# Kernel tuning notes

Hardware: AMD Instinct MI355X
Metric: run time of the kernel (lower is better)

## Reference

```python
import jax, jax.numpy as jnp
import numpy as np
import math

H = 16
D_MODEL = 1024
D_K = D_MODEL // H


def setup_inputs() -> dict:
    key = jax.random.key(0)
    ks = jax.random.split(key, 11)
    B, S = 2, 2048
    scale = 1.0 / math.sqrt(D_MODEL)
    inp = {
        "query": jax.random.normal(ks[0], (B, S, D_MODEL), dtype=jnp.float32),
        "key": jax.random.normal(ks[1], (B, S, D_MODEL), dtype=jnp.float32),
        "value": jax.random.normal(ks[2], (B, S, D_MODEL), dtype=jnp.float32),
        # torch nn.Linear convention: W is [out_features, in_features]
        "Wq": jax.random.normal(ks[3], (D_MODEL, D_MODEL), dtype=jnp.float32) * scale,
        "bq": jnp.zeros((D_MODEL,), dtype=jnp.float32),
        "Wk": jax.random.normal(ks[4], (D_MODEL, D_MODEL), dtype=jnp.float32) * scale,
        "bk": jnp.zeros((D_MODEL,), dtype=jnp.float32),
        "Wv": jax.random.normal(ks[5], (D_MODEL, D_MODEL), dtype=jnp.float32) * scale,
        "bv": jnp.zeros((D_MODEL,), dtype=jnp.float32),
        "Wo": jax.random.normal(ks[6], (D_MODEL, D_MODEL), dtype=jnp.float32) * scale,
        "bo": jnp.zeros((D_MODEL,), dtype=jnp.float32),
    }
    return inp


def _split_heads(x):
    # [b, s, h*d_k] -> [b, h, s, d_k]
    b, s, _ = x.shape
    return x.reshape(b, s, H, D_K).transpose(0, 2, 1, 3)


def reference(query, key, value, Wq, bq, Wk, bk, Wv, bv, Wo, bo):
    q = _split_heads(query @ Wq.T + bq)
    k = _split_heads(key @ Wk.T + bk)
    v = _split_heads(value @ Wv.T + bv)
    # scaled dot-product attention, full L x L scores per head
    scores = jnp.einsum("bhqd,bhkd->bhqk", q, k) / math.sqrt(D_K)
    attn = jax.nn.softmax(scores, axis=-1)
    ctx = jnp.einsum("bhqk,bhkd->bhqd", attn, v)  # [b, h, s, d_k]
    b, h, s, d = ctx.shape
    ctx = ctx.transpose(0, 2, 1, 3).reshape(b, s, h * d)
    return ctx @ Wo.T + bo
```

## Files before the change

### kernel.cpp

```cpp
#include <hip/hip_runtime.h>

typedef unsigned int u32;
typedef unsigned short u16;
typedef __attribute__((ext_vector_type(8))) short short8;
typedef __attribute__((ext_vector_type(4))) float f32x4;
typedef __attribute__((ext_vector_type(2))) u32 u32x2;
typedef __attribute__((ext_vector_type(4))) u32 u32x4;

#define DEV __device__ __forceinline__

DEV u16 f2bf(float f) {
  u32 u = __builtin_bit_cast(u32, f);
  u = (u + 0x7FFFu + ((u >> 16) & 1u)) >> 16;
  return (u16)u;
}

DEV float fexp2(float x) {
#if __has_builtin(__builtin_amdgcn_exp2f)
  return __builtin_amdgcn_exp2f(x);
#else
  return exp2f(x);
#endif
}

DEV u32 cvt_pk_bf16(float lo, float hi) {
  u32 r;
  asm("v_cvt_pk_bf16_f32 %0, %1, %2" : "=v"(r) : "v"(lo), "v"(hi));
  return r;
}

DEV void llds16(const void* g, void* lds) {
  __builtin_amdgcn_global_load_lds(
      (const __attribute__((address_space(1))) u32*)g,
      (__attribute__((address_space(3))) u32*)lds, 16, 0, 0);
}

struct CvtArgs {
  const float* src[7];
  u16* dst[7];
};

__global__ void cvt_all(CvtArgs ca) {
  int i = blockIdx.x * blockDim.x + threadIdx.x;
  int chunk = i >> 17;
  int seg = chunk < 12 ? (chunk >> 2) : (chunk - 9);
  u32 base8 = (seg < 3) ? (u32)seg * 524288u : 1572864u + ((u32)seg - 3) * 131072u;
  size_t off = ((size_t)i - base8) * 8;
  const f32x4* p = (const f32x4*)(ca.src[seg] + off);
  f32x4 a = p[0], b = p[1];
  short8 o;
  o[0] = (short)f2bf(a[0]); o[1] = (short)f2bf(a[1]);
  o[2] = (short)f2bf(a[2]); o[3] = (short)f2bf(a[3]);
  o[4] = (short)f2bf(b[0]); o[5] = (short)f2bf(b[1]);
  o[6] = (short)f2bf(b[2]); o[7] = (short)f2bf(b[3]);
  *(short8*)(ca.dst[seg] + off) = o;
}

struct GemmArgs {
  const u16* A[3];
  const u16* W[3];
  const float* bias[3];
  void* C[3];
  float scale[3];
};

template <int BM, int BN, int WAVES_M, int OUT_BF16, int NB_M>
__global__ __launch_bounds__(256, 2) void gemm_bt(GemmArgs ga) {
  constexpr int K = 1024, N = 1024;
  constexpr int WAVES_N = 4 / WAVES_M;
  constexpr int WM = BM / WAVES_M, WN = BN / WAVES_N;
  constexpr int AM = WM / 16, AN = WN / 16;
  constexpr int SEGS = (BM + BN) / 16;
  constexpr int PW = SEGS / 4;

  __shared__ u16 lsA[BM * 32];
  __shared__ u16 lsB[BN * 32];

  const u32 orig = blockIdx.x;
  const u32 nid = (orig & 7u) * (gridDim.x >> 3) + (orig >> 3);
  const int bn = (int)(nid & 7u);
  const int bm = (int)((nid >> 3) % (u32)NB_M);
  const int z = (int)((nid >> 3) / (u32)NB_M);

  const u16* __restrict__ A = ga.A[z];
  const u16* __restrict__ W = ga.W[z];
  const int tid = threadIdx.x;
  const int l = tid & 63, w = tid >> 6;
  const int lg = l >> 4, lr = l & 15;
  const int wm = w / WAVES_N, wn = w % WAVES_N;

  f32x4 acc[AM][AN];
#pragma unroll
  for (int i = 0; i < AM; ++i)
#pragma unroll
    for (int j = 0; j < AN; ++j) acc[i][j] = (f32x4){0.f, 0.f, 0.f, 0.f};

  for (int k0 = 0; k0 < K; k0 += 32) {
    __syncthreads();
#pragma unroll
    for (int i = 0; i < PW; ++i) {
      int s = w * PW + i;
      if (s < BM / 16) {
        u32 sb = s * 1024;
        u32 lb = sb + l * 16;
        u32 row = lb >> 6, colS = (lb & 63) >> 1;
        llds16(A + (size_t)(bm * BM + row) * K + k0 + colS, (char*)lsA + sb);
      } else {
        u32 sb = (u32)(s - BM / 16) * 1024;
        u32 lb = sb + l * 16;
        u32 row = lb >> 6, colS = (lb & 63) >> 1;
        llds16(W + (size_t)(bn * BN + row) * K + k0 + colS, (char*)lsB + sb);
      }
    }
    __syncthreads();
    short8 af[AM], bf[AN];
#pragma unroll
    for (int i = 0; i < AM; ++i)
      af[i] = *(const short8*)&lsA[(wm * WM + i * 16 + lr) * 32 + lg * 8];
#pragma unroll
    for (int j = 0; j < AN; ++j)
      bf[j] = *(const short8*)&lsB[(wn * WN + j * 16 + lr) * 32 + lg * 8];
#pragma unroll
    for (int i = 0; i < AM; ++i)
#pragma unroll
      for (int j = 0; j < AN; ++j)
        acc[i][j] = __builtin_amdgcn_mfma_f32_16x16x32_bf16(af[i], bf[j], acc[i][j], 0, 0, 0);
  }

  const float sc = ga.scale[z];
  const float* __restrict__ bias = ga.bias[z];
#pragma unroll
  for (int j = 0; j < AN; ++j) {
    int col = bn * BN + wn * WN + j * 16 + lr;
    float bv = bias[col];
#pragma unroll
    for (int i = 0; i < AM; ++i) {
      int row0 = bm * BM + wm * WM + i * 16 + lg * 4;
#pragma unroll
      for (int r = 0; r < 4; ++r) {
        float v = (acc[i][j][r] + bv) * sc;
        if constexpr (OUT_BF16)
          ((u16*)ga.C[z])[(size_t)(row0 + r) * N + col] = f2bf(v);
        else
          ((float*)ga.C[z])[(size_t)(row0 + r) * N + col] = v;
      }
    }
  }
}

__global__ __launch_bounds__(256, 2) void attn_fwd(
    const u16* __restrict__ Q, const u16* __restrict__ Kp,
    const u16* __restrict__ V, u16* __restrict__ O) {
  constexpr int S = 2048, LD = 1024;
  __shared__ u16 Kt[2][64 * 64];
  __shared__ u16 Vt[2][64 * 64];
  const int tid = threadIdx.x;
  const int l = tid & 63, w = tid >> 6;
  const int lg = l >> 4, lr = l & 15;

  const u32 orig = blockIdx.x;
  const u32 nid = (orig & 7u) * 64u + (orig >> 3);
  const int qt = (int)(nid & 15u);
  const int h = (int)((nid >> 4) & 15u);
  const int b = (int)(nid >> 8);

  const size_t base = ((size_t)b * S) * LD + h * 64;
  const int q0 = qt * 128 + w * 32;

  short8 qf[2][2];
#pragma unroll
  for (int g = 0; g < 2; ++g)
#pragma unroll
    for (int c = 0; c < 2; ++c)
      qf[g][c] = *(const short8*)&Q[base + (size_t)(q0 + g * 16 + lr) * LD + c * 32 + lg * 8];

  f32x4 acc[2][4];
#pragma unroll
  for (int g = 0; g < 2; ++g)
#pragma unroll
    for (int i = 0; i < 4; ++i) acc[g][i] = (f32x4){0.f, 0.f, 0.f, 0.f};
  float lsum[2] = {0.f, 0.f};

  const int m = tid & 31;
  const int kp0 = m * 2;
  const int key0 = ((m & 16) << 1) + ((m & 2) << 3) + (((m >> 2) & 3) << 2) + ((m & 1) << 1);
  const int vd0 = (tid >> 5) * 8;

#define KSTAGE(T, BUF)                                                          \
  {                                                                             \
    _Pragma("unroll") for (int i_ = 0; i_ < 2; ++i_) {                          \
      u32 sb = (u32)(w * 2 + i_) * 1024;                                        \
      u32 lb = sb + l * 16;                                                     \
      u32 key = lb >> 7;                                                        \
      u32 inner = (lb & 127) ^ ((key & 7) << 4);                                \
      llds16(Kp + base + (size_t)((T) * 64 + key) * LD + (inner >> 1),          \
             (char*)Kt[BUF] + sb);                                              \
    }                                                                           \
  }
#define VWRITE(BUF, VA, VB)                                                     \
  {                                                                             \
    _Pragma("unroll") for (int jj = 0; jj < 8; ++jj) {                          \
      u32 pv = (u32)(u16)(VA)[jj] | ((u32)(u16)(VB)[jj] << 16);                 \
      u32 addr = (u32)((vd0 + jj) * 128 + kp0 * 2) ^ ((u32)jj << 4);            \
      *(u32*)((char*)Vt[BUF] + addr) = pv;                                      \
    }                                                                           \
  }

  {
    short8 va = *(const short8*)&V[base + (size_t)key0 * LD + vd0];
    short8 vb = *(const short8*)&V[base + (size_t)(key0 + 1) * LD + vd0];
    KSTAGE(0, 0);
    VWRITE(0, va, vb);
  }
  __syncthreads();

  int cur = 0;
  for (int t = 0; t < 32; ++t) {
    const int kb = t * 64;
    short8 nva, nvb;
    if (t < 31) {
      nva = *(const short8*)&V[base + (size_t)(kb + 64 + key0) * LD + vd0];
      nvb = *(const short8*)&V[base + (size_t)(kb + 64 + key0 + 1) * LD + vd0];
      KSTAGE(t + 1, cur ^ 1);
    }

    f32x4 sv[2][4];
    __builtin_amdgcn_s_setprio(1);
#pragma unroll
    for (int ks = 0; ks < 4; ++ks) {
      u32 a0 = (u32)(((ks * 16 + lr) * 128 + lg * 16) ^ ((lr & 7) << 4));
      short8 kf0 = *(const short8*)((const char*)Kt[cur] + a0);
      short8 kf1 = *(const short8*)((const char*)Kt[cur] + (a0 ^ 64));
#pragma unroll
      for (int g = 0; g < 2; ++g) {
        f32x4 s = (f32x4){0.f, 0.f, 0.f, 0.f};
        s = __builtin_amdgcn_mfma_f32_16x16x32_bf16(kf0, qf[g][0], s, 0, 0, 0);
        s = __builtin_amdgcn_mfma_f32_16x16x32_bf16(kf1, qf[g][1], s, 0, 0, 0);
        sv[g][ks] = s;
      }
    }
    __builtin_amdgcn_s_setprio(0);

    u32 pk[2][8];
#pragma unroll
    for (int g = 0; g < 2; ++g) {
#pragma unroll
      for (int ks = 0; ks < 4; ++ks) {
        float e0 = fexp2(sv[g][ks][0]), e1 = fexp2(sv[g][ks][1]);
        float e2 = fexp2(sv[g][ks][2]), e3 = fexp2(sv[g][ks][3]);
        lsum[g] += (e0 + e1) + (e2 + e3);
        pk[g][ks * 2 + 0] = cvt_pk_bf16(e0, e1);
        pk[g][ks * 2 + 1] = cvt_pk_bf16(e2, e3);
      }
    }

    __builtin_amdgcn_s_setprio(1);
#pragma unroll
    for (int ds = 0; ds < 4; ++ds) {
#pragma unroll
      for (int c = 0; c < 2; ++c) {
        u32 va_ = (u32)(((ds * 16 + lr) * 128 + c * 64 + lg * 16) ^ ((lr & 7) << 4));
        short8 vf = *(const short8*)((const char*)Vt[cur] + va_);
#pragma unroll
        for (int g = 0; g < 2; ++g) {
          u32x4 pc = {pk[g][c * 4 + 0], pk[g][c * 4 + 1], pk[g][c * 4 + 2], pk[g][c * 4 + 3]};
          short8 pf = __builtin_bit_cast(short8, pc);
          acc[g][ds] = __builtin_amdgcn_mfma_f32_16x16x32_bf16(vf, pf, acc[g][ds], 0, 0, 0);
        }
      }
    }
    __builtin_amdgcn_s_setprio(0);

    if (t < 31) VWRITE(cur ^ 1, nva, nvb);
    __syncthreads();
    cur ^= 1;
  }

#pragma unroll
  for (int g = 0; g < 2; ++g) {
    lsum[g] += __shfl_xor(lsum[g], 16);
    lsum[g] += __shfl_xor(lsum[g], 32);
  }
#pragma unroll
  for (int g = 0; g < 2; ++g) {
    float inv = __builtin_amdgcn_rcpf(lsum[g]);
#pragma unroll
    for (int ds = 0; ds < 4; ++ds) {
      u32x2 ov;
      ov[0] = cvt_pk_bf16(acc[g][ds][0] * inv, acc[g][ds][1] * inv);
      ov[1] = cvt_pk_bf16(acc[g][ds][2] * inv, acc[g][ds][3] * inv);
      *(u32x2*)&O[base + (size_t)(q0 + g * 16 + lr) * LD + ds * 16 + lg * 4] = ov;
    }
  }
#undef KSTAGE
#undef VWRITE
}

extern "C" void kernel_launch(void* const* d_in, const int* in_sizes, int n_in,
                              void* d_out, int out_size, void* d_ws, size_t ws_size,
                              hipStream_t stream) {
  constexpr size_t SZ_X = 4096ull * 1024;
  constexpr size_t SZ_W = 1024ull * 1024;
  const float* bq = (const float*)d_in[4];
  const float* bk = (const float*)d_in[6];
  const float* bv = (const float*)d_in[8];
  const float* bo = (const float*)d_in[10];

  char* ws = (char*)d_ws;
  u16* xq = (u16*)ws;
  u16* xk = xq + SZ_X;
  u16* xv = xk + SZ_X;
  u16* wqb = xv + SZ_X;
  u16* wkb = wqb + SZ_W;
  u16* wvb = wkb + SZ_W;
  u16* wob = wvb + SZ_W;
  u16* Qp = wob + SZ_W;
  u16* Kp = Qp + SZ_X;
  u16* Vp = Kp + SZ_X;
  u16* Cx = Vp + SZ_X;

  CvtArgs ca;
  ca.src[0] = (const float*)d_in[0]; ca.dst[0] = xq;
  ca.src[1] = (const float*)d_in[1]; ca.dst[1] = xk;
  ca.src[2] = (const float*)d_in[2]; ca.dst[2] = xv;
  ca.src[3] = (const float*)d_in[3]; ca.dst[3] = wqb;
  ca.src[4] = (const float*)d_in[5]; ca.dst[4] = wkb;
  ca.src[5] = (const float*)d_in[7]; ca.dst[5] = wvb;
  ca.src[6] = (const float*)d_in[9]; ca.dst[6] = wob;
  cvt_all<<<dim3(8192), 256, 0, stream>>>(ca);

  GemmArgs g1;
  g1.A[0] = xq;  g1.A[1] = xk;  g1.A[2] = xv;
  g1.W[0] = wqb; g1.W[1] = wkb; g1.W[2] = wvb;
  g1.bias[0] = bq; g1.bias[1] = bk; g1.bias[2] = bv;
  g1.C[0] = Qp; g1.C[1] = Kp; g1.C[2] = Vp;
  g1.scale[0] = 0.18033688011112042f;
  g1.scale[1] = 1.f; g1.scale[2] = 1.f;
  gemm_bt<128, 128, 2, 1, 32><<<dim3(768), 256, 0, stream>>>(g1);

  attn_fwd<<<dim3(512), 256, 0, stream>>>(Qp, Kp, Vp, Cx);

  GemmArgs g2 = {};
  g2.A[0] = Cx; g2.W[0] = wob; g2.bias[0] = bo; g2.C[0] = d_out; g2.scale[0] = 1.f;
  gemm_bt<64, 128, 1, 0, 64><<<dim3(512), 256, 0, stream>>>(g2);
}
```

Measured before the change: 126.8 us.

## Software-pipeline attention loop with 4-deep K/V LDS ring and QK lookahead

```diff
diff --git a/kernel.cpp b/kernel.cpp
--- a/kernel.cpp
+++ b/kernel.cpp
@@ -152,8 +152,8 @@
     const u16* __restrict__ Q, const u16* __restrict__ Kp,
     const u16* __restrict__ V, u16* __restrict__ O) {
   constexpr int S = 2048, LD = 1024;
-  __shared__ u16 Kt[2][64 * 64];
-  __shared__ u16 Vt[2][64 * 64];
+  __shared__ u16 Kt[4][64 * 64];
+  __shared__ u16 Vt[4][64 * 64];
   const int tid = threadIdx.x;
   const int l = tid & 63, w = tid >> 6;
   const int lg = l >> 4, lr = l & 15;
@@ -186,7 +186,7 @@
   const int key0 = ((m & 16) << 1) + ((m & 2) << 3) + (((m >> 2) & 3) << 2) + ((m & 1) << 1);
   const int vd0 = (tid >> 5) * 8;
 
-#define KSTAGE(T, BUF)                                                          \
+#define KSTAGE(T)                                                               \
   {                                                                             \
     _Pragma("unroll") for (int i_ = 0; i_ < 2; ++i_) {                          \
       u32 sb = (u32)(w * 2 + i_) * 1024;                                        \
@@ -194,86 +194,89 @@
       u32 key = lb >> 7;                                                        \
       u32 inner = (lb & 127) ^ ((key & 7) << 4);                                \
       llds16(Kp + base + (size_t)((T) * 64 + key) * LD + (inner >> 1),          \
-             (char*)Kt[BUF] + sb);                                              \
-    }                                                                           \
-  }
-#define VWRITE(BUF, VA, VB)                                                     \
+             (char*)Kt[(T) & 3] + sb);                                          \
+    }                                                                           \
+  }
+#define VLOAD(T, VA, VB)                                                        \
+  {                                                                             \
+    VA = *(const short8*)&V[base + (size_t)((T) * 64 + key0) * LD + vd0];       \
+    VB = *(const short8*)&V[base + (size_t)((T) * 64 + key0 + 1) * LD + vd0];   \
+  }
+#define VWRITE(T, VA, VB)                                                       \
   {                                                                             \
     _Pragma("unroll") for (int jj = 0; jj < 8; ++jj) {                          \
       u32 pv = (u32)(u16)(VA)[jj] | ((u32)(u16)(VB)[jj] << 16);                 \
       u32 addr = (u32)((vd0 + jj) * 128 + kp0 * 2) ^ ((u32)jj << 4);            \
-      *(u32*)((char*)Vt[BUF] + addr) = pv;                                      \
-    }                                                                           \
-  }
-
-  {
-    short8 va = *(const short8*)&V[base + (size_t)key0 * LD + vd0];
-    short8 vb = *(const short8*)&V[base + (size_t)(key0 + 1) * LD + vd0];
-    KSTAGE(0, 0);
-    VWRITE(0, va, vb);
-  }
+      *(u32*)((char*)Vt[(T) & 3] + addr) = pv;                                  \
+    }                                                                           \
+  }
+#define QK(T, SV)                                                               \
+  {                                                                             \
+    __builtin_amdgcn_s_setprio(1);                                              \
+    _Pragma("unroll") for (int ks = 0; ks < 4; ++ks) {                          \
+      u32 a0 = (u32)(((ks * 16 + lr) * 128 + lg * 16) ^ ((lr & 7) << 4));       \
+      short8 kf0 = *(const short8*)((const char*)Kt[(T) & 3] + a0);             \
+      short8 kf1 = *(const short8*)((const char*)Kt[(T) & 3] + (a0 ^ 64));      \
+      _Pragma("unroll") for (int g = 0; g < 2; ++g) {                           \
+        f32x4 s_ = (f32x4){0.f, 0.f, 0.f, 0.f};                                 \
+        s_ = __builtin_amdgcn_mfma_f32_16x16x32_bf16(kf0, qf[g][0], s_, 0, 0, 0); \
+        s_ = __builtin_amdgcn_mfma_f32_16x16x32_bf16(kf1, qf[g][1], s_, 0, 0, 0); \
+        SV[g][ks] = s_;                                                         \
+      }                                                                         \
+    }                                                                           \
+    __builtin_amdgcn_s_setprio(0);                                              \
+  }
+#define SM(SV, PK)                                                              \
+  {                                                                             \
+    _Pragma("unroll") for (int g = 0; g < 2; ++g) {                             \
+      _Pragma("unroll") for (int ks = 0; ks < 4; ++ks) {                        \
+        float e0 = fexp2(SV[g][ks][0]), e1 = fexp2(SV[g][ks][1]);               \
+        float e2 = fexp2(SV[g][ks][2]), e3 = fexp2(SV[g][ks][3]);               \
+        lsum[g] += (e0 + e1) + (e2 + e3);                                       \
+        PK[g][ks * 2 + 0] = cvt_pk_bf16(e0, e1);                                \
+        PK[g][ks * 2 + 1] = cvt_pk_bf16(e2, e3);                                \
+      }                                                                         \
+    }                                                                           \
+  }
+#define PV(T, PK)                                                               \
+  {                                                                             \
+    __builtin_amdgcn_s_setprio(1);                                              \
+    _Pragma("unroll") for (int ds = 0; ds < 4; ++ds) {                          \
+      _Pragma("unroll") for (int c = 0; c < 2; ++c) {                           \
+        u32 va_ = (u32)(((ds * 16 + lr) * 128 + c * 64 + lg * 16) ^ ((lr & 7) << 4)); \
+        short8 vf = *(const short8*)((const char*)Vt[(T) & 3] + va_);           \
+        _Pragma("unroll") for (int g = 0; g < 2; ++g) {                         \
+          u32x4 pc = {PK[g][c * 4 + 0], PK[g][c * 4 + 1], PK[g][c * 4 + 2], PK[g][c * 4 + 3]}; \
+          short8 pf = __builtin_bit_cast(short8, pc);                           \
+          acc[g][ds] = __builtin_amdgcn_mfma_f32_16x16x32_bf16(vf, pf, acc[g][ds], 0, 0, 0); \
+        }                                                                       \
+      }                                                                         \
+    }                                                                           \
+    __builtin_amdgcn_s_setprio(0);                                              \
+  }
+#define ITER(t, SVC, SVN, VCA, VCB, VNA, VNB)                                   \
+  {                                                                             \
+    if ((t) < 30) { VLOAD((t) + 2, VNA, VNB); KSTAGE((t) + 2); }                \
+    if ((t) < 31) QK((t) + 1, SVN);                                             \
+    u32 pk_[2][8];                                                              \
+    SM(SVC, pk_);                                                               \
+    if ((t) < 31) VWRITE((t) + 1, VCA, VCB);                                    \
+    PV(t, pk_);                                                                 \
+    __syncthreads();                                                            \
+  }
+
+  f32x4 svA[2][4], svB[2][4];
+  short8 vaA, vbA, vaB, vbB;
+
+  VLOAD(0, vaB, vbB); KSTAGE(0);
+  VLOAD(1, vaA, vbA); KSTAGE(1);
+  VWRITE(0, vaB, vbB);
   __syncthreads();
-
-  int cur = 0;
-  for (int t = 0; t < 32; ++t) {
-    const int kb = t * 64;
-    short8 nva, nvb;
-    if (t < 31) {
-      nva = *(const short8*)&V[base + (size_t)(kb + 64 + key0) * LD + vd0];
-      nvb = *(const short8*)&V[base + (size_t)(kb + 64 + key0 + 1) * LD + vd0];
-      KSTAGE(t + 1, cur ^ 1);
-    }
-
-    f32x4 sv[2][4];
-    __builtin_amdgcn_s_setprio(1);
-#pragma unroll
-    for (int ks = 0; ks < 4; ++ks) {
-      u32 a0 = (u32)(((ks * 16 + lr) * 128 + lg * 16) ^ ((lr & 7) << 4));
-      short8 kf0 = *(const short8*)((const char*)Kt[cur] + a0);
-      short8 kf1 = *(const short8*)((const char*)Kt[cur] + (a0 ^ 64));
-#pragma unroll
-      for (int g = 0; g < 2; ++g) {
-        f32x4 s = (f32x4){0.f, 0.f, 0.f, 0.f};
-        s = __builtin_amdgcn_mfma_f32_16x16x32_bf16(kf0, qf[g][0], s, 0, 0, 0);
-        s = __builtin_amdgcn_mfma_f32_16x16x32_bf16(kf1, qf[g][1], s, 0, 0, 0);
-        sv[g][ks] = s;
-      }
-    }
-    __builtin_amdgcn_s_setprio(0);
-
-    u32 pk[2][8];
-#pragma unroll
-    for (int g = 0; g < 2; ++g) {
-#pragma unroll
-      for (int ks = 0; ks < 4; ++ks) {
-        float e0 = fexp2(sv[g][ks][0]), e1 = fexp2(sv[g][ks][1]);
-        float e2 = fexp2(sv[g][ks][2]), e3 = fexp2(sv[g][ks][3]);
-        lsum[g] += (e0 + e1) + (e2 + e3);
-        pk[g][ks * 2 + 0] = cvt_pk_bf16(e0, e1);
-        pk[g][ks * 2 + 1] = cvt_pk_bf16(e2, e3);
-      }
-    }
-
-    __builtin_amdgcn_s_setprio(1);
-#pragma unroll
-    for (int ds = 0; ds < 4; ++ds) {
-#pragma unroll
-      for (int c = 0; c < 2; ++c) {
-        u32 va_ = (u32)(((ds * 16 + lr) * 128 + c * 64 + lg * 16) ^ ((lr & 7) << 4));
-        short8 vf = *(const short8*)((const char*)Vt[cur] + va_);
-#pragma unroll
-        for (int g = 0; g < 2; ++g) {
-          u32x4 pc = {pk[g][c * 4 + 0], pk[g][c * 4 + 1], pk[g][c * 4 + 2], pk[g][c * 4 + 3]};
-          short8 pf = __builtin_bit_cast(short8, pc);
-          acc[g][ds] = __builtin_amdgcn_mfma_f32_16x16x32_bf16(vf, pf, acc[g][ds], 0, 0, 0);
-        }
-      }
-    }
-    __builtin_amdgcn_s_setprio(0);
-
-    if (t < 31) VWRITE(cur ^ 1, nva, nvb);
-    __syncthreads();
-    cur ^= 1;
+  QK(0, svA);
+
+  for (int tt = 0; tt < 16; ++tt) {
+    ITER(2 * tt, svA, svB, vaA, vbA, vaB, vbB);
+    ITER(2 * tt + 1, svB, svA, vaB, vbB, vaA, vbA);
   }
 
 #pragma unroll
@@ -293,7 +296,12 @@
     }
   }
 #undef KSTAGE
+#undef VLOAD
 #undef VWRITE
+#undef QK
+#undef SM
+#undef PV
+#undef ITER
 }
 
 extern "C" void kernel_launch(void* const* d_in, const int* in_sizes, int n_in,
```

Measured after the change: 127.2 us. Within noise of the previous version (+0.3%).
